# Performance work log

Measured on AMD Instinct MI355X. Metric: run time of the kernel, lower is better.

The kernel has to match this reference:

```python
import jax, jax.numpy as jnp
import numpy as np

KH = KW = 3
STRIDE = 1
ITERATIONS = 2
EPS = 1e-7


def _squash(s):
    # squash along last axis (capsule dim)
    sn = jnp.sum(s * s, axis=-1, keepdims=True)
    return (sn / (1.0 + sn)) * s / jnp.sqrt(sn + EPS)


def setup_inputs() -> dict:
    key = jax.random.key(0)
    k1, k2 = jax.random.split(key)
    x = jax.random.normal(k1, (4, 14, 14, 32, 8), dtype=jnp.float32)
    # W: [1,1,1,filters_out, caps_per_patch=3*3*32, dims_out=16, dims_in=8], stddev=0.1 init
    W = 0.1 * jax.random.normal(k2, (1, 1, 1, 32, 288, 16, 8), dtype=jnp.float32)
    return {"x": x, "W": W}


def reference(x, W):
    B, H, Wd, Fin, Din = x.shape
    Ho = (H - KH) // STRIDE + 1
    Wo = (Wd - KW) // STRIDE + 1
    # Patch extraction, channel order (kh, kw, Fin) to match tf.image.extract_patches
    patches = jnp.stack(
        [x[:, i:i + Ho * STRIDE:STRIDE, j:j + Wo * STRIDE:STRIDE]
         for i in range(KH) for j in range(KW)],
        axis=3,
    )  # [B,Ho,Wo,KH*KW,Fin,Din]
    patches = patches.reshape(B, Ho, Wo, KH * KW * Fin, Din)  # [B,Ho,Wo,C,Di]

    Wm = W[0, 0, 0]  # [F, C, Do, Di]
    F, C, Do, _ = Wm.shape
    # predictions[b,h,w,f,c,o] = sum_i W[f,c,o,i] * patches[b,h,w,c,i]
    preds = jnp.einsum('fcoi,bhwci->bhwfco', Wm, patches)

    logits = jnp.zeros((B, Ho, Wo, F, C), dtype=preds.dtype)
    outputs = jnp.zeros((B, Ho, Wo, F, Do), dtype=preds.dtype)
    for _ in range(ITERATIONS):
        # agreement = predictions^T @ outputs over the dims_out axis
        agreement = jnp.einsum('bhwfco,bhwfo->bhwfc', preds, outputs)
        logits = logits + agreement
        # NOTE: original code softmaxes over axis=3 (the filters_out axis)
        cc = jax.nn.softmax(logits, axis=3)  # [B,Ho,Wo,F,C]
        centroids = jnp.sum(cc[..., None] * preds, axis=4)  # [B,Ho,Wo,F,Do]
        outputs = _squash(centroids)
    return outputs
```

## Files before the change

kernel.cpp:

```cpp
#include <hip/hip_runtime.h>

#define NB   4
#define H_IN 14
#define W_IN 14
#define FIN  32
#define DI   8
#define F    32
#define C    288
#define DO   16
#define HO   12
#define WO   12
#define NPOS (NB*HO*WO)
#define EPS  1e-7f

#define CH   16
#define CC   (C/CH)
#define GRID2 ((CH*NPOS)/4)

#define KTOT (C*DI)
#define KPAD 2312

#define W2H_BYTES  ((size_t)F*C*DO*DI*2)
#define WH_BYTES   ((size_t)F*C*DO*DI*2)
#define PH_BYTES   ((size_t)NPOS*KTOT*2)
#define PART_BYTES ((size_t)CH*NPOS*F*DO*4)
#define OUT1_BYTES ((size_t)NPOS*F*DO*4)

#define CVT_W2H 576
#define CVT_WH  576
#define CVT_PH  648
#define CVT_GRID (CVT_W2H + CVT_WH + CVT_PH)

typedef _Float16 h2 __attribute__((ext_vector_type(2)));
typedef _Float16 h8v __attribute__((ext_vector_type(8)));
typedef float    f4v __attribute__((ext_vector_type(4)));

__device__ __forceinline__ unsigned int pack2(float a, float b) {
    h2 v; v.x = (_Float16)a; v.y = (_Float16)b;
    return __builtin_bit_cast(unsigned int, v);
}

__device__ __forceinline__ float dot8h(const uint4 w, const uint4 v, float acc) {
#if __has_builtin(__builtin_amdgcn_fdot2)
    acc = __builtin_amdgcn_fdot2(__builtin_bit_cast(h2, w.x), __builtin_bit_cast(h2, v.x), acc, false);
    acc = __builtin_amdgcn_fdot2(__builtin_bit_cast(h2, w.y), __builtin_bit_cast(h2, v.y), acc, false);
    acc = __builtin_amdgcn_fdot2(__builtin_bit_cast(h2, w.z), __builtin_bit_cast(h2, v.z), acc, false);
    acc = __builtin_amdgcn_fdot2(__builtin_bit_cast(h2, w.w), __builtin_bit_cast(h2, v.w), acc, false);
#else
    const h2 w0 = __builtin_bit_cast(h2, w.x), v0 = __builtin_bit_cast(h2, v.x);
    const h2 w1 = __builtin_bit_cast(h2, w.y), v1 = __builtin_bit_cast(h2, v.y);
    const h2 w2 = __builtin_bit_cast(h2, w.z), v2 = __builtin_bit_cast(h2, v.z);
    const h2 w3 = __builtin_bit_cast(h2, w.w), v3 = __builtin_bit_cast(h2, v.w);
    acc += (float)w0.x*(float)v0.x + (float)w0.y*(float)v0.y
         + (float)w1.x*(float)v1.x + (float)w1.y*(float)v1.y
         + (float)w2.x*(float)v2.x + (float)w2.y*(float)v2.y
         + (float)w3.x*(float)v3.x + (float)w3.y*(float)v3.y;
#endif
    return acc;
}

__device__ __forceinline__ int xbase_of(int pos) {
    const int b = pos/(HO*WO), rem = pos%(HO*WO), ho = rem/WO, wo = rem%WO;
    return ((b*H_IN + ho)*W_IN + wo)*FIN*DI;
}

__device__ __forceinline__ int coff_of(int c) {
    const int slab = c >> 5, fin = c & 31;
    const int kh = slab/3, kw = slab%3;
    return (kh*W_IN + kw)*FIN*DI + fin*DI;
}

__global__ __launch_bounds__(256) void kernConv(const float* __restrict__ Wt,
                                                const float* __restrict__ x,
                                                unsigned short* __restrict__ W2h,
                                                unsigned short* __restrict__ Wh,
                                                unsigned short* __restrict__ Ph) {
    const int b = blockIdx.x;
    if (b < CVT_W2H) {
        const int idx = b*256 + threadIdx.x;
        const float* src = Wt + (size_t)idx*8;
        const float4 a = *(const float4*)src;
        const float4 bb = *(const float4*)(src + 4);
        uint4 r;
        r.x = pack2(a.x, a.y);   r.y = pack2(a.z, a.w);
        r.z = pack2(bb.x, bb.y); r.w = pack2(bb.z, bb.w);
        const int o = idx & 15;
        const int c = (idx >> 4) % C;
        const int f = idx / (C*DO);
        ((uint4*)W2h)[(size_t)(c*DO + o)*F + f] = r;
    } else if (b < CVT_W2H + CVT_WH) {
        const int idx = (b - CVT_W2H)*256 + threadIdx.x;
        const float* src = Wt + (size_t)idx*8;
        const float4 a = *(const float4*)src;
        const float4 bb = *(const float4*)(src + 4);
        uint4 r;
        r.x = pack2(a.x, a.y);   r.y = pack2(a.z, a.w);
        r.z = pack2(bb.x, bb.y); r.w = pack2(bb.z, bb.w);
        ((uint4*)Wh)[idx] = r;
    } else {
        const int pc = (b - CVT_W2H - CVT_WH)*256 + threadIdx.x;
        const int pos = pc / C, c = pc % C;
        const float* src = x + xbase_of(pos) + coff_of(c);
        const float4 a = *(const float4*)src;
        const float4 bb = *(const float4*)(src + 4);
        uint4 r;
        r.x = pack2(a.x, a.y);   r.y = pack2(a.z, a.w);
        r.z = pack2(bb.x, bb.y); r.w = pack2(bb.z, bb.w);
        ((uint4*)Ph)[pc] = r;
    }
}

__global__ __launch_bounds__(512) void kernM1(const unsigned short* __restrict__ Ph,
                                              const unsigned short* __restrict__ Wh,
                                              float* __restrict__ out1)
{
    __shared__ unsigned short As[16][KPAD];
    __shared__ f4v red2[4][64];

    const int tid  = threadIdx.x;
    const int lane = tid & 63;
    const int wv   = tid >> 6;
    const int pt   = blockIdx.x >> 3;
    const int fg   = blockIdx.x & 7;
    const int f    = (wv & 3)*8 + fg;
    const int ks   = wv >> 2;
    const int pos0 = pt*16;
    const int n    = lane & 15, q = lane >> 4;

    #pragma unroll
    for (int r = 0; r < 9; ++r) {
        const int linear = r*512 + tid;
        const int row = linear / 288, col8 = linear % 288;
        const uint4 v = *(const uint4*)(Ph + (size_t)(pos0 + row)*KTOT + col8*8);
        *(uint4*)&As[row][col8*8] = v;
    }
    __syncthreads();

    const unsigned short* pa = &As[n][q*8];
    const unsigned short* pb = Wh + ((size_t)(f*C + q)*DO + n)*DI;

    f4v acc0 = {0.f,0.f,0.f,0.f}, acc1 = {0.f,0.f,0.f,0.f};
    const int s0 = ks*36;
    #pragma unroll 4
    for (int s = s0; s < s0 + 36; s += 2) {
        const h8v a0 = *(const h8v*)(pa + s*32);
        const h8v b0 = *(const h8v*)(pb + (size_t)s*4*DO*DI);
        const h8v a1 = *(const h8v*)(pa + (s+1)*32);
        const h8v b1 = *(const h8v*)(pb + (size_t)(s+1)*4*DO*DI);
        acc0 = __builtin_amdgcn_mfma_f32_16x16x32_f16(a0, b0, acc0, 0, 0, 0);
        acc1 = __builtin_amdgcn_mfma_f32_16x16x32_f16(a1, b1, acc1, 0, 0, 0);
    }

    f4v tot;
    #pragma unroll
    for (int r = 0; r < 4; ++r) tot[r] = acc0[r] + acc1[r];

    if (wv >= 4) red2[wv - 4][lane] = tot;
    __syncthreads();

    if (wv < 4) {
        const f4v other = red2[wv][lane];
        #pragma unroll
        for (int r = 0; r < 4; ++r) {
            const float v = (tot[r] + other[r]) * (1.f/32.f);
            float sq = v*v;
            sq += __shfl_xor(sq, 1);
            sq += __shfl_xor(sq, 2);
            sq += __shfl_xor(sq, 4);
            sq += __shfl_xor(sq, 8);
            const float sc = (sq/(1.f + sq)) * rsqrtf(sq + EPS);
            out1[(size_t)(pos0 + q*4 + r)*512 + f*DO + n] = v * sc;
        }
    }
}

__global__ __launch_bounds__(256) void kern2w(const unsigned short* __restrict__ Ph,
                                              const unsigned short* __restrict__ W2h,
                                              const float* __restrict__ out1,
                                              float* __restrict__ part2)
{
    const int tid  = threadIdx.x;
    const int lane = tid & 63;
    const int wv   = tid >> 6;
    const int f    = lane & 31;
    const int og   = lane >> 5;
    const int o0   = og*8;

    const int ch   = blockIdx.x & (CH-1);
    const int gq   = blockIdx.x >> 4;
    const int pos  = __builtin_amdgcn_readfirstlane(gq*4 + wv);

    const int c0 = ch*CC;
    const uint4* W2h4 = (const uint4*)W2h;

    float u[8];
    {
        const float* up = out1 + (size_t)pos*512 + f*DO + o0;
        const float4 a = *(const float4*)up;
        const float4 b = *(const float4*)(up + 4);
        u[0]=a.x; u[1]=a.y; u[2]=a.z; u[3]=a.w;
        u[4]=b.x; u[5]=b.y; u[6]=b.z; u[7]=b.w;
    }

    float acc[8];
    #pragma unroll
    for (int k = 0; k < 8; ++k) acc[k] = 0.f;

    #pragma unroll 2
    for (int cl = 0; cl < CC; ++cl) {
        const int c = c0 + cl;

        const uint4 xv = *(const uint4*)(Ph + (size_t)pos*KTOT + c*DI);

        float pred[8];
        #pragma unroll
        for (int k = 0; k < 8; ++k) {
            const uint4 w = W2h4[(size_t)(c*DO + o0 + k)*F + f];
            pred[k] = dot8h(w, xv, 0.f);
        }

        float ap = 0.f;
        #pragma unroll
        for (int k = 0; k < 8; ++k) ap += pred[k]*u[k];
        ap += __shfl_xor(ap, 32);

        float m = ap;
        m = fmaxf(m, __shfl_xor(m, 1));
        m = fmaxf(m, __shfl_xor(m, 2));
        m = fmaxf(m, __shfl_xor(m, 4));
        m = fmaxf(m, __shfl_xor(m, 8));
        m = fmaxf(m, __shfl_xor(m, 16));
        const float e = __expf(ap - m);
        float s = e;
        s += __shfl_xor(s, 1);
        s += __shfl_xor(s, 2);
        s += __shfl_xor(s, 4);
        s += __shfl_xor(s, 8);
        s += __shfl_xor(s, 16);
        const float cc = e / s;

        #pragma unroll
        for (int k = 0; k < 8; ++k) acc[k] += cc*pred[k];
    }

    float* dst = part2 + ((size_t)(ch*NPOS + pos)*F + f)*DO + o0;
    float4 s0, s1;
    s0.x=acc[0]; s0.y=acc[1]; s0.z=acc[2]; s0.w=acc[3];
    s1.x=acc[4]; s1.y=acc[5]; s1.z=acc[6]; s1.w=acc[7];
    *(float4*)dst = s0;
    *(float4*)(dst + 4) = s1;
}

__global__ __launch_bounds__(64) void kern3(const float* __restrict__ part2,
                                            float* __restrict__ out)
{
    const int lane = threadIdx.x;
    const int pos  = blockIdx.x;
    const int f = lane & 31, oh = lane >> 5, o0 = oh*8;

    float c0x=0.f,c0y=0.f,c0z=0.f,c0w=0.f, c1x=0.f,c1y=0.f,c1z=0.f,c1w=0.f;
    #pragma unroll
    for (int k = 0; k < CH; ++k) {
        const float* s = part2 + ((size_t)(k*NPOS + pos)*F + f)*DO + o0;
        const float4 a = *(const float4*)s;
        const float4 b = *(const float4*)(s + 4);
        c0x+=a.x; c0y+=a.y; c0z+=a.z; c0w+=a.w;
        c1x+=b.x; c1y+=b.y; c1z+=b.z; c1w+=b.w;
    }
    float sq = c0x*c0x + c0y*c0y + c0z*c0z + c0w*c0w
             + c1x*c1x + c1y*c1y + c1z*c1z + c1w*c1w;
    sq += __shfl_xor(sq, 32);
    const float sc = (sq/(1.f + sq)) * rsqrtf(sq + EPS);

    float* dst = out + ((size_t)pos*F + f)*DO + o0;
    float4 s0, s1;
    s0.x=c0x*sc; s0.y=c0y*sc; s0.z=c0z*sc; s0.w=c0w*sc;
    s1.x=c1x*sc; s1.y=c1y*sc; s1.z=c1z*sc; s1.w=c1w*sc;
    *(float4*)dst = s0;
    *(float4*)(dst + 4) = s1;
}

__device__ __forceinline__ float dot8(const float4* __restrict__ w,
                                      const float4 p0, const float4 p1) {
    float4 a = w[0], b = w[1];
    return a.x*p0.x + a.y*p0.y + a.z*p0.z + a.w*p0.w
         + b.x*p1.x + b.y*p1.y + b.z*p1.z + b.w*p1.w;
}

__global__ __launch_bounds__(256) void capsule_kernel_f32(
    const float* __restrict__ x, const float* __restrict__ Wt,
    float* __restrict__ out)
{
    __shared__ float patch[C*DI];
    __shared__ float cent[F*DO];
    __shared__ float out1[F*DO];
    __shared__ float agr[F*C];
    __shared__ float scale_s[F];

    const int tid = threadIdx.x;
    const int pos = blockIdx.x;
    const int b   = pos / (HO*WO);
    const int rem = pos % (HO*WO);
    const int ho  = rem / WO;
    const int wo  = rem % WO;

    #pragma unroll
    for (int slab = 0; slab < 9; ++slab) {
        const int kh = slab / 3, kw = slab % 3;
        const float* src = x + (((b*H_IN + ho + kh)*W_IN + (wo + kw))*FIN)*DI;
        patch[slab*256 + tid] = src[tid];
    }
    __syncthreads();

    const float4* pv = (const float4*)patch;

    {
        const int fo0 = tid, fo1 = tid + 256;
        const int f0 = fo0 >> 4, o0 = fo0 & 15;
        const int f1 = fo1 >> 4, o1 = fo1 & 15;
        float acc0 = 0.f, acc1 = 0.f;
        for (int c = 0; c < C; ++c) {
            const float4 p0 = pv[c*2], p1 = pv[c*2+1];
            acc0 += dot8((const float4*)(Wt + ((f0*C + c)*DO + o0)*DI), p0, p1);
            acc1 += dot8((const float4*)(Wt + ((f1*C + c)*DO + o1)*DI), p0, p1);
        }
        cent[fo0] = acc0 * (1.f/32.f);
        cent[fo1] = acc1 * (1.f/32.f);
    }
    __syncthreads();

    if (tid < F) {
        float sn = 0.f;
        #pragma unroll
        for (int o = 0; o < DO; ++o) { float v = cent[tid*DO + o]; sn += v*v; }
        const float sc = (sn/(1.f + sn)) * rsqrtf(sn + EPS);
        #pragma unroll
        for (int o = 0; o < DO; ++o) out1[tid*DO + o] = cent[tid*DO + o] * sc;
    }
    __syncthreads();

    #pragma unroll 1
    for (int r = 0; r < (F*C)/256; ++r) {
        const int pp = tid + 256*r;
        const int f = pp / C, c = pp % C;
        const float4* wrow = (const float4*)(Wt + (f*C + c)*DO*DI);
        const float4 p0 = pv[c*2], p1 = pv[c*2+1];
        float a = 0.f;
        #pragma unroll
        for (int o = 0; o < DO; ++o) a += dot8(wrow + o*2, p0, p1) * out1[f*DO + o];
        agr[pp] = a;
    }
    __syncthreads();

    for (int c = tid; c < C; c += 256) {
        float m = -1e30f;
        #pragma unroll
        for (int f = 0; f < F; ++f) m = fmaxf(m, agr[f*C + c]);
        float s = 0.f;
        #pragma unroll
        for (int f = 0; f < F; ++f) {
            const float e = __expf(agr[f*C + c] - m);
            agr[f*C + c] = e; s += e;
        }
        const float inv = 1.f / s;
        #pragma unroll
        for (int f = 0; f < F; ++f) agr[f*C + c] *= inv;
    }
    __syncthreads();

    {
        const int fo0 = tid, fo1 = tid + 256;
        const int f0 = fo0 >> 4, o0 = fo0 & 15;
        const int f1 = fo1 >> 4, o1 = fo1 & 15;
        float acc0 = 0.f, acc1 = 0.f;
        for (int c = 0; c < C; ++c) {
            const float4 p0 = pv[c*2], p1 = pv[c*2+1];
            acc0 += agr[f0*C + c] * dot8((const float4*)(Wt + ((f0*C + c)*DO + o0)*DI), p0, p1);
            acc1 += agr[f1*C + c] * dot8((const float4*)(Wt + ((f1*C + c)*DO + o1)*DI), p0, p1);
        }
        cent[fo0] = acc0;
        cent[fo1] = acc1;
    }
    __syncthreads();

    if (tid < F) {
        float sn = 0.f;
        #pragma unroll
        for (int o = 0; o < DO; ++o) { float v = cent[tid*DO + o]; sn += v*v; }
        scale_s[tid] = (sn/(1.f + sn)) * rsqrtf(sn + EPS);
    }
    __syncthreads();

    out[pos*(F*DO) + tid]       = cent[tid]       * scale_s[tid >> 4];
    out[pos*(F*DO) + tid + 256] = cent[tid + 256] * scale_s[(tid >> 4) + 16];
}

extern "C" void kernel_launch(void* const* d_in, const int* in_sizes, int n_in,
                              void* d_out, int out_size, void* d_ws, size_t ws_size,
                              hipStream_t stream) {
    const float* x  = (const float*)d_in[0];
    const float* Wt = (const float*)d_in[1];
    float* out = (float*)d_out;

    if (ws_size >= W2H_BYTES + WH_BYTES + PH_BYTES + PART_BYTES + OUT1_BYTES) {
        char* p = (char*)d_ws;
        unsigned short* W2h = (unsigned short*)p;            p += W2H_BYTES;
        unsigned short* Wh  = (unsigned short*)p;            p += WH_BYTES;
        unsigned short* Ph  = (unsigned short*)p;            p += PH_BYTES;
        float* part = (float*)p;                             p += PART_BYTES;
        float* out1 = (float*)p;

        kernConv<<<CVT_GRID, 256, 0, stream>>>(Wt, x, W2h, Wh, Ph);
        kernM1<<<36*8, 512, 0, stream>>>(Ph, Wh, out1);
        kern2w<<<GRID2, 256, 0, stream>>>(Ph, W2h, out1, part);
        kern3<<<NPOS, 64, 0, stream>>>(part, out);
    } else {
        capsule_kernel_f32<<<NPOS, 256, 0, stream>>>(x, Wt, out);
    }
}
```

Before: 130.1 us.

## Stage per-capsule weights in double-buffered LDS and process two positions per wave

The second routing kernel now has each wave handle two spatial positions, so every weight vector feeds two dot products, and the grid is halved. The 8 KB weight slab for each input capsule is loaded cooperatively into shared memory with double buffering and read from LDS instead of being fetched from global memory by every wave. This cuts global/L2 weight traffic, at the cost of a __syncthreads per capsule iteration, more registers, and fewer blocks to fill the GPU.

```diff
diff --git a/kernel.cpp b/kernel.cpp
--- a/kernel.cpp
+++ b/kernel.cpp
@@ -15,7 +15,8 @@
 
 #define CH   16
 #define CC   (C/CH)
-#define GRID2 ((CH*NPOS)/4)
+#define GP   2
+#define GRID2 ((CH*NPOS/GP)/4)
 
 #define KTOT (C*DI)
 #define KPAD 2312
@@ -179,6 +180,8 @@
                                               const float* __restrict__ out1,
                                               float* __restrict__ part2)
 {
+    __shared__ uint4 Ws[2][512];
+
     const int tid  = threadIdx.x;
     const int lane = tid & 63;
     const int wv   = tid >> 6;
@@ -188,67 +191,91 @@
 
     const int ch   = blockIdx.x & (CH-1);
     const int gq   = blockIdx.x >> 4;
-    const int pos  = __builtin_amdgcn_readfirstlane(gq*4 + wv);
+    const int grp  = __builtin_amdgcn_readfirstlane(gq*4 + wv);
+    const int pos0 = grp*GP;
 
     const int c0 = ch*CC;
     const uint4* W2h4 = (const uint4*)W2h;
 
-    float u[8];
-    {
-        const float* up = out1 + (size_t)pos*512 + f*DO + o0;
+    float u[8][GP];
+    #pragma unroll
+    for (int p = 0; p < GP; ++p) {
+        const float* up = out1 + (size_t)(pos0 + p)*512 + f*DO + o0;
         const float4 a = *(const float4*)up;
         const float4 b = *(const float4*)(up + 4);
-        u[0]=a.x; u[1]=a.y; u[2]=a.z; u[3]=a.w;
-        u[4]=b.x; u[5]=b.y; u[6]=b.z; u[7]=b.w;
-    }
-
-    float acc[8];
-    #pragma unroll
-    for (int k = 0; k < 8; ++k) acc[k] = 0.f;
-
-    #pragma unroll 2
+        u[0][p]=a.x; u[1][p]=a.y; u[2][p]=a.z; u[3][p]=a.w;
+        u[4][p]=b.x; u[5][p]=b.y; u[6][p]=b.z; u[7][p]=b.w;
+    }
+
+    float acc[8][GP];
+    #pragma unroll
+    for (int k = 0; k < 8; ++k)
+        #pragma unroll
+        for (int p = 0; p < GP; ++p) acc[k][p] = 0.f;
+
+    Ws[0][tid]       = W2h4[(size_t)c0*512 + tid];
+    Ws[0][tid + 256] = W2h4[(size_t)c0*512 + tid + 256];
+
+    #pragma unroll 1
     for (int cl = 0; cl < CC; ++cl) {
+        __syncthreads();
+        const int buf = cl & 1;
+        if (cl + 1 < CC) {
+            const size_t cb = (size_t)(c0 + cl + 1)*512;
+            Ws[buf^1][tid]       = W2h4[cb + tid];
+            Ws[buf^1][tid + 256] = W2h4[cb + tid + 256];
+        }
         const int c = c0 + cl;
 
-        const uint4 xv = *(const uint4*)(Ph + (size_t)pos*KTOT + c*DI);
-
-        float pred[8];
+        uint4 xv[GP];
+        #pragma unroll
+        for (int p = 0; p < GP; ++p)
+            xv[p] = *(const uint4*)(Ph + (size_t)(pos0 + p)*KTOT + c*DI);
+
+        float pred[8][GP];
         #pragma unroll
         for (int k = 0; k < 8; ++k) {
-            const uint4 w = W2h4[(size_t)(c*DO + o0 + k)*F + f];
-            pred[k] = dot8h(w, xv, 0.f);
-        }
-
-        float ap = 0.f;
-        #pragma unroll
-        for (int k = 0; k < 8; ++k) ap += pred[k]*u[k];
-        ap += __shfl_xor(ap, 32);
-
-        float m = ap;
-        m = fmaxf(m, __shfl_xor(m, 1));
-        m = fmaxf(m, __shfl_xor(m, 2));
-        m = fmaxf(m, __shfl_xor(m, 4));
-        m = fmaxf(m, __shfl_xor(m, 8));
-        m = fmaxf(m, __shfl_xor(m, 16));
-        const float e = __expf(ap - m);
-        float s = e;
-        s += __shfl_xor(s, 1);
-        s += __shfl_xor(s, 2);
-        s += __shfl_xor(s, 4);
-        s += __shfl_xor(s, 8);
-        s += __shfl_xor(s, 16);
-        const float cc = e / s;
-
-        #pragma unroll
-        for (int k = 0; k < 8; ++k) acc[k] += cc*pred[k];
-    }
-
-    float* dst = part2 + ((size_t)(ch*NPOS + pos)*F + f)*DO + o0;
-    float4 s0, s1;
-    s0.x=acc[0]; s0.y=acc[1]; s0.z=acc[2]; s0.w=acc[3];
-    s1.x=acc[4]; s1.y=acc[5]; s1.z=acc[6]; s1.w=acc[7];
-    *(float4*)dst = s0;
-    *(float4*)(dst + 4) = s1;
+            const uint4 w = Ws[buf][(o0 + k)*32 + f];
+            #pragma unroll
+            for (int p = 0; p < GP; ++p) pred[k][p] = dot8h(w, xv[p], 0.f);
+        }
+
+        #pragma unroll
+        for (int p = 0; p < GP; ++p) {
+            float ap = 0.f;
+            #pragma unroll
+            for (int k = 0; k < 8; ++k) ap += pred[k][p]*u[k][p];
+            ap += __shfl_xor(ap, 32);
+
+            float m = ap;
+            m = fmaxf(m, __shfl_xor(m, 1));
+            m = fmaxf(m, __shfl_xor(m, 2));
+            m = fmaxf(m, __shfl_xor(m, 4));
+            m = fmaxf(m, __shfl_xor(m, 8));
+            m = fmaxf(m, __shfl_xor(m, 16));
+            const float e = __expf(ap - m);
+            float s = e;
+            s += __shfl_xor(s, 1);
+            s += __shfl_xor(s, 2);
+            s += __shfl_xor(s, 4);
+            s += __shfl_xor(s, 8);
+            s += __shfl_xor(s, 16);
+            const float cc = e / s;
+
+            #pragma unroll
+            for (int k = 0; k < 8; ++k) acc[k][p] += cc*pred[k][p];
+        }
+    }
+
+    #pragma unroll
+    for (int p = 0; p < GP; ++p) {
+        float* dst = part2 + ((size_t)(ch*NPOS + pos0 + p)*F + f)*DO + o0;
+        float4 s0, s1;
+        s0.x=acc[0][p]; s0.y=acc[1][p]; s0.z=acc[2][p]; s0.w=acc[3][p];
+        s1.x=acc[4][p]; s1.y=acc[5][p]; s1.z=acc[6][p]; s1.w=acc[7][p];
+        *(float4*)dst = s0;
+        *(float4*)(dst + 4) = s1;
+    }
 }
 
 __global__ __launch_bounds__(64) void kern3(const float* __restrict__ part2,
```

Result: faster. 125.0 us (-3.9%).
